# Performance work log

Hardware: AMD Instinct MI355X
Metric: run time of the kernel (lower is better)

## Reference

```python
import jax, jax.numpy as jnp
import numpy as np

EPS = 1e-6

def setup_inputs() -> dict:
    key = jax.random.key(0)
    k1, k2, k3 = jax.random.split(key, 3)
    B, N, D, K = 8, 4096, 512, 8
    x = jax.random.normal(k1, (B, N, D), dtype=jnp.float32)
    W = jax.random.normal(k2, (D, K), dtype=jnp.float32) * (1.0 / np.sqrt(D))
    b = jnp.zeros((K,), dtype=jnp.float32)
    eps = jax.random.normal(k3, (B, K, D), dtype=jnp.float32)
    return {"x": x, "W": W, "b": b, "eps": eps}

def reference(x, W, b, eps):
    # x: [B,N,D], W: [D,K], b: [K], eps: [B,K,D]
    logits = jnp.einsum('bnd,dk->bnk', x, W) + b          # [B,N,K]
    probs = jax.nn.softmax(logits, axis=-1)               # softmax over clusters
    p = jnp.swapaxes(probs, 1, 2)                         # [B,K,N]
    # weighted sums (NOT normalized over N, matching the original)
    mu_k = jnp.einsum('bkn,bnd->bkd', p, x)               # [B,K,D]
    diff = x[:, None, :, :] - mu_k[:, :, None, :]         # [B,K,N,D]
    sigma_k = jnp.einsum('bkn,bknd->bkd', p, diff * diff) # [B,K,D]
    z_k = mu_k + eps * jnp.sqrt(sigma_k + EPS)            # reparameterization
    kl = -0.5 * jnp.sum(1.0 + jnp.log(sigma_k + EPS) - mu_k * mu_k - sigma_k, axis=-1)  # [B,K]
    kl_loss = jnp.mean(kl)
    pooled_z = jnp.mean(z_k, axis=1)                      # [B,D]
    return pooled_z, kl_loss
```

## Files before the change

kernel.cpp:

```cpp
#include <hip/hip_runtime.h>


typedef float v2f __attribute__((ext_vector_type(2)));

#define B_ 8
#define N_ 4096
#define D_ 512
#define K_ 8
#define EPS_ 1e-6f
#define CHUNKS 64
#define ROWS_PB 64
#define PART_FLOATS(cs) ((size_t)B_ * (cs) * K_ * D_ * 2)

__global__ __launch_bounds__(512, 2)
void k1_fused(const float* __restrict__ x, const float* __restrict__ W,
              const float* __restrict__ bias, float* __restrict__ partial,
              float* __restrict__ s0g, int cstride, int atomic_mode) {
#pragma clang fp contract(fast)
  const int lane = threadIdx.x & 63;
  const int wave = threadIdx.x >> 6;
  const int b     = blockIdx.x >> 6;
  const int chunk = blockIdx.x & 63;

  __shared__ float p_lds[ROWS_PB][K_];
  __shared__ v2f   comb[4][16][64];
  __shared__ float s0sh[8][K_];

  const float* xb = x + ((size_t)b * N_ + (size_t)chunk * ROWS_PB) * D_;

  {
    v2f wk[8][4];
#pragma unroll
    for (int dj = 0; dj < 8; ++dj) {
      const float4* wr = reinterpret_cast<const float4*>(&W[(8 * lane + dj) * K_]);
      float4 wa = wr[0], wb4 = wr[1];
      wk[dj][0] = (v2f){wa.x, wa.y};  wk[dj][1] = (v2f){wa.z, wa.w};
      wk[dj][2] = (v2f){wb4.x, wb4.y}; wk[dj][3] = (v2f){wb4.z, wb4.w};
    }
    const float biasv = bias[lane & 7];
    const bool c0 = (lane & 1) != 0;
    const bool c1 = (lane & 2) != 0;
    const bool c2 = (lane & 4) != 0;

    float s0acc = 0.f;
    for (int j = 0; j < 8; ++j) {
      const int row = wave * 8 + j;
      const float4* xr = reinterpret_cast<const float4*>(&xb[(size_t)row * D_]);
      float4 xa = xr[2 * lane];
      float4 xc = xr[2 * lane + 1];
      float xv[8] = {xa.x, xa.y, xa.z, xa.w, xc.x, xc.y, xc.z, xc.w};

      v2f qp[4] = {(v2f){0,0},(v2f){0,0},(v2f){0,0},(v2f){0,0}};
#pragma unroll
      for (int dj = 0; dj < 8; ++dj) {
        v2f xx = (v2f){xv[dj], xv[dj]};
#pragma unroll
        for (int kp = 0; kp < 4; ++kp) qp[kp] += wk[dj][kp] * xx;
      }
      float q0=qp[0].x,q1=qp[0].y,q2=qp[1].x,q3=qp[1].y;
      float q4=qp[2].x,q5=qp[2].y,q6=qp[3].x,q7=qp[3].y;

      float r0 = c0 ? q0 : q1, r1 = c0 ? q2 : q3, r2 = c0 ? q4 : q5, r3 = c0 ? q6 : q7;
      r0 = __shfl_xor(r0, 1, 64); r1 = __shfl_xor(r1, 1, 64);
      r2 = __shfl_xor(r2, 1, 64); r3 = __shfl_xor(r3, 1, 64);
      float a0 = (c0 ? q1 : q0) + r0, a1 = (c0 ? q3 : q2) + r1;
      float a2 = (c0 ? q5 : q4) + r2, a3 = (c0 ? q7 : q6) + r3;
      float sg0 = c1 ? a0 : a1, sg1 = c1 ? a2 : a3;
      sg0 = __shfl_xor(sg0, 2, 64); sg1 = __shfl_xor(sg1, 2, 64);
      float b0 = (c1 ? a1 : a0) + sg0, b1 = (c1 ? a3 : a2) + sg1;
      float g0 = c2 ? b0 : b1;
      g0 = __shfl_xor(g0, 4, 64);
      float t = (c2 ? b1 : b0) + g0;
      t += __shfl_xor(t, 8, 64);
      t += __shfl_xor(t, 16, 64);
      t += __shfl_xor(t, 32, 64);
      t += biasv;

      float mx = fmaxf(t, __shfl_xor(t, 1, 64));
      mx = fmaxf(mx, __shfl_xor(mx, 2, 64));
      mx = fmaxf(mx, __shfl_xor(mx, 4, 64));
      float e = __expf(t - mx);
      float se = e + __shfl_xor(e, 1, 64);
      se += __shfl_xor(se, 2, 64);
      se += __shfl_xor(se, 4, 64);
      float pm = e * __builtin_amdgcn_rcpf(se);

      s0acc += pm;
      if (lane < K_) p_lds[row][lane] = pm;
    }
    if (lane < K_) s0sh[wave][lane] = s0acc;
  }
  __syncthreads();

  if (threadIdx.x < K_) {
    float s = 0.f;
#pragma unroll
    for (int w = 0; w < 8; ++w) s += s0sh[w][threadIdx.x];
    atomicAdd(s0g + b * K_ + threadIdx.x, s);
  }

  const int q = wave & 3;
  const int h = wave >> 2;
  const int rbase = h * 32;

  v2f acc[8][2];
#pragma unroll
  for (int dj = 0; dj < 8; ++dj) { acc[dj][0] = (v2f){0,0}; acc[dj][1] = (v2f){0,0}; }

  const float4* xr0 = reinterpret_cast<const float4*>(&xb[(size_t)rbase * D_]);
  float4 xa = xr0[2 * lane];
  float4 xc = xr0[2 * lane + 1];
  v2f pk = *reinterpret_cast<const v2f*>(&p_lds[rbase][2 * q]);

  for (int r = 0; r < 32; ++r) {
    const int nr = rbase + ((r + 1 < 32) ? r + 1 : r);
    const float4* xrn = reinterpret_cast<const float4*>(&xb[(size_t)nr * D_]);
    float4 na = xrn[2 * lane];
    float4 nc = xrn[2 * lane + 1];
    v2f npk = *reinterpret_cast<const v2f*>(&p_lds[nr][2 * q]);

    float xv[8] = {xa.x, xa.y, xa.z, xa.w, xc.x, xc.y, xc.z, xc.w};
    v2f p0 = (v2f){pk.x, pk.x};
    v2f p1 = (v2f){pk.y, pk.y};
#pragma unroll
    for (int dj = 0; dj < 8; ++dj) {
      v2f m2 = (v2f){xv[dj], xv[dj] * xv[dj]};
      acc[dj][0] += m2 * p0;
      acc[dj][1] += m2 * p1;
    }
    xa = na; xc = nc; pk = npk;
  }

  if (h == 1) {
#pragma unroll
    for (int dj = 0; dj < 8; ++dj) {
      comb[q][dj * 2 + 0][lane] = acc[dj][0];
      comb[q][dj * 2 + 1][lane] = acc[dj][1];
    }
  }
  __syncthreads();

  if (h == 0) {
    const int cslot = atomic_mode ? 0 : chunk;
#pragma unroll
    for (int kk = 0; kk < 2; ++kk) {
      const int k = 2 * q + kk;
      float* dst = partial + (((size_t)(b * cstride + cslot) * K_ + k) * D_ + 8 * lane) * 2;
#pragma unroll
      for (int g = 0; g < 4; ++g) {
        v2f u0 = acc[2 * g][kk]     + comb[q][(2 * g) * 2 + kk][lane];
        v2f u1 = acc[2 * g + 1][kk] + comb[q][(2 * g + 1) * 2 + kk][lane];
        if (atomic_mode) {
          atomicAdd(dst + g * 4 + 0, u0.x); atomicAdd(dst + g * 4 + 1, u0.y);
          atomicAdd(dst + g * 4 + 2, u1.x); atomicAdd(dst + g * 4 + 3, u1.y);
        } else {
          float4 v; v.x = u0.x; v.y = u0.y; v.z = u1.x; v.w = u1.y;
          *reinterpret_cast<float4*>(dst + g * 4) = v;
        }
      }
    }
  }
}

__global__ __launch_bounds__(256)
void k2_final(const float* __restrict__ partial, const float* __restrict__ s0g,
              const float* __restrict__ eps, float* __restrict__ out,
              int cstride, int nchunks) {
  const int b = blockIdx.x >> 5;
  const int slice = blockIdx.x & 31;
  const int tid = threadIdx.x;
  const int cq = tid >> 7;
  const int k  = (tid >> 4) & 7;
  const int dl = tid & 15;
  const int d  = slice * 16 + dl;

  __shared__ v2f red2[2][K_][16];
  __shared__ float zsh[K_][16];
  __shared__ float klsh[4];

  const int half = (nchunks + 1) >> 1;
  const int cbeg = cq * half;
  const int cend = (cbeg + half < nchunks) ? (cbeg + half) : nchunks;

  const float* base = partial + (((size_t)b * cstride) * K_ + k) * D_ * 2 + d * 2;
  const size_t cstep = (size_t)K_ * D_ * 2;

  v2f s0v = (v2f){0,0}, s1v = (v2f){0,0}, s2v = (v2f){0,0}, s3v = (v2f){0,0};
  int c = cbeg;
  for (; c + 4 <= cend; c += 4) {
    s0v += *reinterpret_cast<const v2f*>(base + (size_t)c * cstep);
    s1v += *reinterpret_cast<const v2f*>(base + (size_t)(c + 1) * cstep);
    s2v += *reinterpret_cast<const v2f*>(base + (size_t)(c + 2) * cstep);
    s3v += *reinterpret_cast<const v2f*>(base + (size_t)(c + 3) * cstep);
  }
  for (; c < cend; ++c) s0v += *reinterpret_cast<const v2f*>(base + (size_t)c * cstep);
  red2[cq][k][dl] = (s0v + s1v) + (s2v + s3v);
  __syncthreads();

  float klp = 0.f;
  if (cq == 0) {
    v2f sv = red2[0][k][dl] + red2[1][k][dl];
    const float S1 = sv.x, S2 = sv.y;
    const float S0 = s0g[b * K_ + k];
    float sigraw = S2 + (S0 - 2.f) * S1 * S1;
    float sig = fmaxf(sigraw, 0.f) + EPS_;
    float z = S1 + eps[((size_t)(b * K_ + k)) * D_ + d] * sqrtf(sig);
    zsh[k][dl] = z;
    klp = 1.f + logf(sig) - S1 * S1 - sigraw;
  }

  klp += __shfl_xor(klp, 1, 64);
  klp += __shfl_xor(klp, 2, 64);
  klp += __shfl_xor(klp, 4, 64);
  klp += __shfl_xor(klp, 8, 64);
  klp += __shfl_xor(klp, 16, 64);
  klp += __shfl_xor(klp, 32, 64);
  const int lane = tid & 63, wv = tid >> 6;
  if (lane == 0) klsh[wv] = klp;
  __syncthreads();

  if (tid < 16) {
    float pooled = 0.f;
#pragma unroll
    for (int kk = 0; kk < K_; ++kk) pooled += zsh[kk][tid];
    out[b * D_ + slice * 16 + tid] = pooled * 0.125f;
  }
  if (tid == 0) {
    atomicAdd(out + B_ * D_, (klsh[0] + klsh[1] + klsh[2] + klsh[3]) * (-0.5f / (B_ * K_)));
  }
}

extern "C" void kernel_launch(void* const* d_in, const int* in_sizes, int n_in,
                              void* d_out, int out_size, void* d_ws, size_t ws_size,
                              hipStream_t stream) {
  const float* x    = (const float*)d_in[0];
  const float* W    = (const float*)d_in[1];
  const float* bias = (const float*)d_in[2];
  const float* eps  = (const float*)d_in[3];
  float* out = (float*)d_out;
  float* ws  = (float*)d_ws;

  const size_t full_floats = PART_FLOATS(CHUNKS) + B_ * K_;
  const int atomic_mode = (ws_size < full_floats * sizeof(float)) ? 1 : 0;
  const int cstride = atomic_mode ? 1 : CHUNKS;
  const int nchunks = atomic_mode ? 1 : CHUNKS;

  float* partial = ws;
  float* s0g     = partial + PART_FLOATS(cstride);

  if (atomic_mode) {
    hipMemsetAsync(partial, 0, (PART_FLOATS(1) + B_ * K_) * sizeof(float), stream);
  } else {
    hipMemsetAsync(s0g, 0, B_ * K_ * sizeof(float), stream);
  }
  hipMemsetAsync(out + B_ * D_, 0, sizeof(float), stream);

  k1_fused<<<B_ * CHUNKS, 512, 0, stream>>>(x, W, bias, partial, s0g, cstride, atomic_mode);
  k2_final<<<B_ * 32, 256, 0, stream>>>(partial, s0g, eps, out, cstride, nchunks);
}
```

Measured before the change: 52.09 us.

## Halve rows per block, drop intra-block combine, shorten softmax shuffle reduction

Blocks now cover 32 rows with 4 waves instead of 64 rows with 8, giving 1024 blocks. Each wave handles a cluster pair (q, q+4) over all rows, so the shared-memory combine stage and its second barrier go away. The logits reduction now carries two clusters per lane pair, which cuts shuffle steps, and rows are processed in pairs to expose more ILP. The cost is twice as many partial slabs written and then read by the final kernel, which adds HBM traffic in the k2 reduction.

```diff
diff --git a/kernel.cpp b/kernel.cpp
--- a/kernel.cpp
+++ b/kernel.cpp
@@ -8,23 +8,22 @@
 #define D_ 512
 #define K_ 8
 #define EPS_ 1e-6f
-#define CHUNKS 64
-#define ROWS_PB 64
+#define CHUNKS 128
+#define ROWS_PB 32
 #define PART_FLOATS(cs) ((size_t)B_ * (cs) * K_ * D_ * 2)
 
-__global__ __launch_bounds__(512, 2)
+__global__ __launch_bounds__(256, 2)
 void k1_fused(const float* __restrict__ x, const float* __restrict__ W,
               const float* __restrict__ bias, float* __restrict__ partial,
               float* __restrict__ s0g, int cstride, int atomic_mode) {
 #pragma clang fp contract(fast)
   const int lane = threadIdx.x & 63;
   const int wave = threadIdx.x >> 6;
-  const int b     = blockIdx.x >> 6;
-  const int chunk = blockIdx.x & 63;
+  const int b     = blockIdx.x >> 7;
+  const int chunk = blockIdx.x & 127;
 
   __shared__ float p_lds[ROWS_PB][K_];
-  __shared__ v2f   comb[4][16][64];
-  __shared__ float s0sh[8][K_];
+  __shared__ v2f   s0sh[4][4];
 
   const float* xb = x + ((size_t)b * N_ + (size_t)chunk * ROWS_PB) * D_;
 
@@ -34,22 +33,16 @@
     for (int dj = 0; dj < 8; ++dj) {
       const float4* wr = reinterpret_cast<const float4*>(&W[(8 * lane + dj) * K_]);
       float4 wa = wr[0], wb4 = wr[1];
-      wk[dj][0] = (v2f){wa.x, wa.y};  wk[dj][1] = (v2f){wa.z, wa.w};
+      wk[dj][0] = (v2f){wa.x, wa.y};   wk[dj][1] = (v2f){wa.z, wa.w};
       wk[dj][2] = (v2f){wb4.x, wb4.y}; wk[dj][3] = (v2f){wb4.z, wb4.w};
     }
-    const float biasv = bias[lane & 7];
+    const int kq = lane & 3;
+    const v2f biasv2 = (v2f){bias[kq], bias[kq + 4]};
     const bool c0 = (lane & 1) != 0;
     const bool c1 = (lane & 2) != 0;
-    const bool c2 = (lane & 4) != 0;
-
-    float s0acc = 0.f;
-    for (int j = 0; j < 8; ++j) {
-      const int row = wave * 8 + j;
-      const float4* xr = reinterpret_cast<const float4*>(&xb[(size_t)row * D_]);
-      float4 xa = xr[2 * lane];
-      float4 xc = xr[2 * lane + 1];
+
+    auto row_probs = [&](float4 xa, float4 xc) -> v2f {
       float xv[8] = {xa.x, xa.y, xa.z, xa.w, xc.x, xc.y, xc.z, xc.w};
-
       v2f qp[4] = {(v2f){0,0},(v2f){0,0},(v2f){0,0},(v2f){0,0}};
 #pragma unroll
       for (int dj = 0; dj < 8; ++dj) {
@@ -65,98 +58,100 @@
       r2 = __shfl_xor(r2, 1, 64); r3 = __shfl_xor(r3, 1, 64);
       float a0 = (c0 ? q1 : q0) + r0, a1 = (c0 ? q3 : q2) + r1;
       float a2 = (c0 ? q5 : q4) + r2, a3 = (c0 ? q7 : q6) + r3;
-      float sg0 = c1 ? a0 : a1, sg1 = c1 ? a2 : a3;
-      sg0 = __shfl_xor(sg0, 2, 64); sg1 = __shfl_xor(sg1, 2, 64);
-      float b0 = (c1 ? a1 : a0) + sg0, b1 = (c1 ? a3 : a2) + sg1;
-      float g0 = c2 ? b0 : b1;
-      g0 = __shfl_xor(g0, 4, 64);
-      float t = (c2 ? b1 : b0) + g0;
-      t += __shfl_xor(t, 8, 64);
-      t += __shfl_xor(t, 16, 64);
-      t += __shfl_xor(t, 32, 64);
-      t += biasv;
-
-      float mx = fmaxf(t, __shfl_xor(t, 1, 64));
+      float s0_ = c1 ? a0 : a1, s1_ = c1 ? a2 : a3;
+      s0_ = __shfl_xor(s0_, 2, 64); s1_ = __shfl_xor(s1_, 2, 64);
+      v2f t2 = (v2f){(c1 ? a1 : a0) + s0_, (c1 ? a3 : a2) + s1_};
+#pragma unroll
+      for (int m = 4; m <= 32; m <<= 1) {
+        v2f o = (v2f){__shfl_xor(t2.x, m, 64), __shfl_xor(t2.y, m, 64)};
+        t2 += o;
+      }
+      t2 += biasv2;
+      float mx = fmaxf(t2.x, t2.y);
+      mx = fmaxf(mx, __shfl_xor(mx, 1, 64));
       mx = fmaxf(mx, __shfl_xor(mx, 2, 64));
-      mx = fmaxf(mx, __shfl_xor(mx, 4, 64));
-      float e = __expf(t - mx);
-      float se = e + __shfl_xor(e, 1, 64);
+      float ex = __expf(t2.x - mx), ey = __expf(t2.y - mx);
+      float se = ex + ey;
+      se += __shfl_xor(se, 1, 64);
       se += __shfl_xor(se, 2, 64);
-      se += __shfl_xor(se, 4, 64);
-      float pm = e * __builtin_amdgcn_rcpf(se);
-
-      s0acc += pm;
-      if (lane < K_) p_lds[row][lane] = pm;
-    }
-    if (lane < K_) s0sh[wave][lane] = s0acc;
+      float inv = __builtin_amdgcn_rcpf(se);
+      return (v2f){ex * inv, ey * inv};
+    };
+
+    v2f s0acc = (v2f){0.f, 0.f};
+    const int r0w = wave * 8;
+#pragma unroll
+    for (int jp = 0; jp < 4; ++jp) {
+      const int j0 = r0w + 2 * jp;
+      const float4* x0 = reinterpret_cast<const float4*>(&xb[(size_t)j0 * D_]);
+      const float4* x1 = reinterpret_cast<const float4*>(&xb[(size_t)(j0 + 1) * D_]);
+      float4 xa0 = x0[2 * lane], xc0 = x0[2 * lane + 1];
+      float4 xa1 = x1[2 * lane], xc1 = x1[2 * lane + 1];
+      v2f p0 = row_probs(xa0, xc0);
+      v2f p1 = row_probs(xa1, xc1);
+      s0acc += p0 + p1;
+      if (lane < 4) {
+        *reinterpret_cast<v2f*>(&p_lds[j0][2 * lane])     = p0;
+        *reinterpret_cast<v2f*>(&p_lds[j0 + 1][2 * lane]) = p1;
+      }
+    }
+    if (lane < 4) s0sh[wave][lane] = s0acc;
   }
   __syncthreads();
 
-  if (threadIdx.x < K_) {
-    float s = 0.f;
-#pragma unroll
-    for (int w = 0; w < 8; ++w) s += s0sh[w][threadIdx.x];
-    atomicAdd(s0g + b * K_ + threadIdx.x, s);
-  }
-
-  const int q = wave & 3;
-  const int h = wave >> 2;
-  const int rbase = h * 32;
-
-  v2f acc[8][2];
-#pragma unroll
-  for (int dj = 0; dj < 8; ++dj) { acc[dj][0] = (v2f){0,0}; acc[dj][1] = (v2f){0,0}; }
-
-  const float4* xr0 = reinterpret_cast<const float4*>(&xb[(size_t)rbase * D_]);
+  if (threadIdx.x < 4) {
+    v2f s = s0sh[0][threadIdx.x] + s0sh[1][threadIdx.x] +
+            s0sh[2][threadIdx.x] + s0sh[3][threadIdx.x];
+    atomicAdd(s0g + b * K_ + threadIdx.x,     s.x);
+    atomicAdd(s0g + b * K_ + threadIdx.x + 4, s.y);
+  }
+
+  const int q = wave;
+
+  v2f acc0[8], acc1[8];
+#pragma unroll
+  for (int dj = 0; dj < 8; ++dj) { acc0[dj] = (v2f){0,0}; acc1[dj] = (v2f){0,0}; }
+
+  const float4* xr0 = reinterpret_cast<const float4*>(&xb[0]);
   float4 xa = xr0[2 * lane];
   float4 xc = xr0[2 * lane + 1];
-  v2f pk = *reinterpret_cast<const v2f*>(&p_lds[rbase][2 * q]);
-
-  for (int r = 0; r < 32; ++r) {
-    const int nr = rbase + ((r + 1 < 32) ? r + 1 : r);
+  v2f pk = *reinterpret_cast<const v2f*>(&p_lds[0][2 * q]);
+
+  for (int r = 0; r < ROWS_PB; ++r) {
+    const int nr = (r + 1 < ROWS_PB) ? r + 1 : r;
     const float4* xrn = reinterpret_cast<const float4*>(&xb[(size_t)nr * D_]);
     float4 na = xrn[2 * lane];
     float4 nc = xrn[2 * lane + 1];
     v2f npk = *reinterpret_cast<const v2f*>(&p_lds[nr][2 * q]);
 
     float xv[8] = {xa.x, xa.y, xa.z, xa.w, xc.x, xc.y, xc.z, xc.w};
-    v2f p0 = (v2f){pk.x, pk.x};
-    v2f p1 = (v2f){pk.y, pk.y};
+    v2f ps0 = (v2f){pk.x, pk.x};
+    v2f ps1 = (v2f){pk.y, pk.y};
 #pragma unroll
     for (int dj = 0; dj < 8; ++dj) {
       v2f m2 = (v2f){xv[dj], xv[dj] * xv[dj]};
-      acc[dj][0] += m2 * p0;
-      acc[dj][1] += m2 * p1;
+      acc0[dj] += m2 * ps0;
+      acc1[dj] += m2 * ps1;
     }
     xa = na; xc = nc; pk = npk;
   }
 
-  if (h == 1) {
-#pragma unroll
-    for (int dj = 0; dj < 8; ++dj) {
-      comb[q][dj * 2 + 0][lane] = acc[dj][0];
-      comb[q][dj * 2 + 1][lane] = acc[dj][1];
-    }
-  }
-  __syncthreads();
-
-  if (h == 0) {
-    const int cslot = atomic_mode ? 0 : chunk;
-#pragma unroll
-    for (int kk = 0; kk < 2; ++kk) {
-      const int k = 2 * q + kk;
-      float* dst = partial + (((size_t)(b * cstride + cslot) * K_ + k) * D_ + 8 * lane) * 2;
-#pragma unroll
-      for (int g = 0; g < 4; ++g) {
-        v2f u0 = acc[2 * g][kk]     + comb[q][(2 * g) * 2 + kk][lane];
-        v2f u1 = acc[2 * g + 1][kk] + comb[q][(2 * g + 1) * 2 + kk][lane];
-        if (atomic_mode) {
-          atomicAdd(dst + g * 4 + 0, u0.x); atomicAdd(dst + g * 4 + 1, u0.y);
-          atomicAdd(dst + g * 4 + 2, u1.x); atomicAdd(dst + g * 4 + 3, u1.y);
-        } else {
-          float4 v; v.x = u0.x; v.y = u0.y; v.z = u1.x; v.w = u1.y;
-          *reinterpret_cast<float4*>(dst + g * 4) = v;
-        }
+  const int cslot = atomic_mode ? 0 : chunk;
+#pragma unroll
+  for (int kk = 0; kk < 2; ++kk) {
+    const int k = q + 4 * kk;
+    v2f* acc = kk ? acc1 : acc0;
+    float* dst = partial + (((size_t)(b * cstride + cslot) * K_ + k) * D_ + 8 * lane) * 2;
+#pragma unroll
+    for (int g = 0; g < 4; ++g) {
+      v2f u0 = acc[2 * g];
+      v2f u1 = acc[2 * g + 1];
+      if (atomic_mode) {
+        atomicAdd(dst + g * 4 + 0, u0.x); atomicAdd(dst + g * 4 + 1, u0.y);
+        atomicAdd(dst + g * 4 + 2, u1.x); atomicAdd(dst + g * 4 + 3, u1.y);
+      } else {
+        float4 v; v.x = u0.x; v.y = u0.y; v.z = u1.x; v.w = u1.y;
+        *reinterpret_cast<float4*>(dst + g * 4) = v;
       }
     }
   }
@@ -255,6 +250,6 @@
   }
   hipMemsetAsync(out + B_ * D_, 0, sizeof(float), stream);
 
-  k1_fused<<<B_ * CHUNKS, 512, 0, stream>>>(x, W, bias, partial, s0g, cstride, atomic_mode);
+  k1_fused<<<B_ * CHUNKS, 256, 0, stream>>>(x, W, bias, partial, s0g, cstride, atomic_mode);
   k2_final<<<B_ * 32, 256, 0, stream>>>(partial, s0g, eps, out, cstride, nchunks);
 }
```

Measured after the change: 62.26 us. +19.5%, slower.
